# Kernel optimization log

Hardware: AMD Instinct MI355X
Metric: run time of the kernel (lower is better)

The kernel has to match this reference:

```python
import jax, jax.numpy as jnp
import numpy as np
from functools import partial

ALPHA = 0.99   # EMA smoothing factor of unbiasedExponentialSmoother
EPS = 1e-5

def setup_inputs() -> dict:
    key = jax.random.key(0)
    B, C, T = 8, 256, 16384
    x = jax.random.normal(key, (B, C, T), dtype=jnp.float32)
    return {"x": x}

def _causal_unbiased_ema_norm(x, alpha, eps):
    # x: [B, C, T]. Causal instance norm: per (b, c) lane, running unbiased
    # EMA estimates of mean and second moment over time, then normalize.
    B, C, T = x.shape
    xt = jnp.transpose(x, (2, 0, 1))  # [T, B, C] time-major for scan

    def step(carry, xi):
        s1, s2, w = carry
        s1 = alpha * s1 + (1.0 - alpha) * xi          # EMA of x
        s2 = alpha * s2 + (1.0 - alpha) * xi * xi     # EMA of x^2
        w = alpha * w + (1.0 - alpha)                 # bias correction 1-alpha^t
        mean = s1 / w
        var = s2 / w - mean * mean
        out = (xi - mean) * jax.lax.rsqrt(var + eps)
        return (s1, s2, w), out

    z = jnp.zeros((B, C), dtype=x.dtype)
    w0 = jnp.zeros((), dtype=x.dtype)
    _, yt = jax.lax.scan(step, (z, z, w0), xt)
    return jnp.transpose(yt, (1, 2, 0))  # back to [B, C, T]

def reference(x):
    # MyInstanceNorm1d(causal=True, use_unbiasEMA=True, affine=False):
    # permute/unsqueeze wrapper around the causal unbiased-EMA smoother.
    return _causal_unbiased_ema_norm(x, ALPHA, EPS)
```

## Files before the change

kernel.cpp:

```cpp
#include <hip/hip_runtime.h>

#define T_LEN  16384
#define CHUNK  16
#define NTHR   1024
#define NWAVE  (NTHR / 64)

__global__ __launch_bounds__(NTHR, 2)
void ema_norm_kernel(const float* __restrict__ x, float* __restrict__ y) {
    const float A    = 0.99f;
    const float OMA  = (float)(1.0 - 0.99);
    const float EPSF = 1e-5f;
    const float Kf = (float)((double)((float)(1.0 - 0.99)) / (1.0 - (double)0.99f));

    const int row  = blockIdx.x;
    const int tid  = threadIdx.x;
    const int lane = tid & 63;
    const int wid  = tid >> 6;

    const float4* __restrict__ xr =
        reinterpret_cast<const float4*>(x + (size_t)row * T_LEN + (size_t)tid * CHUNK);
    float4* __restrict__ yr =
        reinterpret_cast<float4*>(y + (size_t)row * T_LEN + (size_t)tid * CHUNK);

    float4 xv[4];
#pragma unroll
    for (int i = 0; i < 4; ++i) xv[i] = xr[i];

    float s1 = 0.f, s2 = 0.f;
#pragma unroll
    for (int i = 0; i < 4; ++i) {
        float t;
        t = OMA * xv[i].x; s1 = fmaf(A, s1, t); s2 = fmaf(A, s2, t * xv[i].x);
        t = OMA * xv[i].y; s1 = fmaf(A, s1, t); s2 = fmaf(A, s2, t * xv[i].y);
        t = OMA * xv[i].z; s1 = fmaf(A, s1, t); s2 = fmaf(A, s2, t * xv[i].z);
        t = OMA * xv[i].w; s1 = fmaf(A, s1, t); s2 = fmaf(A, s2, t * xv[i].w);
    }

    float a16 = A;
#pragma unroll
    for (int i = 0; i < 4; ++i) a16 *= a16;
    float d[10];
    d[0] = a16;
#pragma unroll
    for (int k = 1; k < 10; ++k) d[k] = d[k - 1] * d[k - 1];

    float v1 = s1, v2 = s2;
#pragma unroll
    for (int k = 0; k < 6; ++k) {
        const int off = 1 << k;
        float o1 = __shfl_up(v1, off, 64);
        float o2 = __shfl_up(v2, off, 64);
        if (lane >= off) { v1 = fmaf(d[k], o1, v1); v2 = fmaf(d[k], o2, v2); }
    }
    float c1 = __shfl_up(v1, 1, 64);
    float c2 = __shfl_up(v2, 1, 64);
    if (lane == 0) { c1 = 0.f; c2 = 0.f; }

    __shared__ float tot1[NWAVE], tot2[NWAVE];
    if (lane == 63) { tot1[wid] = v1; tot2[wid] = v2; }
    __syncthreads();
    float W1 = 0.f, W2 = 0.f;
    const float Dw = d[6];
    for (int v = 0; v < wid; ++v) {
        W1 = fmaf(W1, Dw, tot1[v]);
        W2 = fmaf(W2, Dw, tot2[v]);
    }
    float fdec = 1.f;
#pragma unroll
    for (int k = 0; k < 6; ++k) if (lane & (1 << k)) fdec *= d[k];
    c1 = fmaf(W1, fdec, c1);
    c2 = fmaf(W2, fdec, c2);

    float pw = 1.f;
#pragma unroll
    for (int k = 0; k < 10; ++k) if (tid & (1 << k)) pw *= d[k];
    float wrun = (tid == 0) ? 0.f : Kf * (1.f - pw);

    s1 = c1; s2 = c2;
#pragma unroll
    for (int i = 0; i < 4; ++i) {
        float4 xq = xv[i];
        float4 oq;
        {   float xi = xq.x; float t = OMA * xi;
            s1 = fmaf(A, s1, t); s2 = fmaf(A, s2, t * xi);
            wrun = fmaf(A, wrun, OMA);
            float invw = 1.0f / wrun;
            float mean = s1 * invw;
            float var  = fmaf(-mean, mean, s2 * invw);
            float rs   = __builtin_amdgcn_rsqf(var + EPSF);
            oq.x = (xi - mean) * rs; }
        {   float xi = xq.y; float t = OMA * xi;
            s1 = fmaf(A, s1, t); s2 = fmaf(A, s2, t * xi);
            wrun = fmaf(A, wrun, OMA);
            float invw = 1.0f / wrun;
            float mean = s1 * invw;
            float var  = fmaf(-mean, mean, s2 * invw);
            float rs   = __builtin_amdgcn_rsqf(var + EPSF);
            oq.y = (xi - mean) * rs; }
        {   float xi = xq.z; float t = OMA * xi;
            s1 = fmaf(A, s1, t); s2 = fmaf(A, s2, t * xi);
            wrun = fmaf(A, wrun, OMA);
            float invw = 1.0f / wrun;
            float mean = s1 * invw;
            float var  = fmaf(-mean, mean, s2 * invw);
            float rs   = __builtin_amdgcn_rsqf(var + EPSF);
            oq.z = (xi - mean) * rs; }
        {   float xi = xq.w; float t = OMA * xi;
            s1 = fmaf(A, s1, t); s2 = fmaf(A, s2, t * xi);
            wrun = fmaf(A, wrun, OMA);
            float invw = 1.0f / wrun;
            float mean = s1 * invw;
            float var  = fmaf(-mean, mean, s2 * invw);
            float rs   = __builtin_amdgcn_rsqf(var + EPSF);
            oq.w = (xi - mean) * rs; }
        yr[i] = oq;
    }
}

extern "C" void kernel_launch(void* const* d_in, const int* in_sizes, int n_in,
                              void* d_out, int out_size, void* d_ws, size_t ws_size,
                              hipStream_t stream) {
    const float* x = (const float*)d_in[0];
    float* y = (float*)d_out;
    const int rows = in_sizes[0] / T_LEN;
    ema_norm_kernel<<<rows, NTHR, 0, stream>>>(x, y);
}
```

Baseline: 239.3 us.

## Process two half-row segments per thread and drop per-step division

Each thread now handles two 16-element chunks, one in each half of the row, with 512-thread blocks instead of 1024. The wave-total carry for the second half is chained across both halves. The output formula is rewritten algebraically as (x*w - s1) * rsqrt(s2*w - s1^2 + eps*w^2), which removes the per-element reciprocal of the running weight. This cuts ALU cost and raises independent work per thread, at the cost of more registers and a longer serial cross-wave loop.

```diff
diff --git a/kernel.cpp b/kernel.cpp
--- a/kernel.cpp
+++ b/kernel.cpp
@@ -1,39 +1,77 @@
 #include <hip/hip_runtime.h>
 
 #define T_LEN  16384
-#define CHUNK  16
-#define NTHR   1024
+#define SUB    16
+#define NTHR   512
 #define NWAVE  (NTHR / 64)
+#define HALF   (T_LEN / 2)
 
-__global__ __launch_bounds__(NTHR, 2)
-void ema_norm_kernel(const float* __restrict__ x, float* __restrict__ y) {
+
+__device__ __forceinline__ void process16(const float4* __restrict__ xv,
+                                          float4* __restrict__ yv,
+                                          float s1, float s2, float w) {
     const float A    = 0.99f;
     const float OMA  = (float)(1.0 - 0.99);
     const float EPSF = 1e-5f;
-    const float Kf = (float)((double)((float)(1.0 - 0.99)) / (1.0 - (double)0.99f));
+#pragma unroll
+    for (int i = 0; i < 4; ++i) {
+        float4 xq = xv[i];
+        float4 oq;
+#pragma unroll
+        for (int e = 0; e < 4; ++e) {
+            float xi = (e == 0) ? xq.x : (e == 1) ? xq.y : (e == 2) ? xq.z : xq.w;
+            float t = OMA * xi;
+            s1 = fmaf(A, s1, t);
+            s2 = fmaf(A, s2, t * xi);
+            w  = fmaf(A, w, OMA);
+            float w2    = w * w;
+            float numer = fmaf(xi, w, -s1);
+            float arg   = fmaf(s2, w, fmaf(-s1, s1, EPSF * w2));
+            float rs    = __builtin_amdgcn_rsqf(arg);
+            float o     = numer * rs;
+            if (e == 0) oq.x = o; else if (e == 1) oq.y = o; else if (e == 2) oq.z = o; else oq.w = o;
+        }
+        yv[i] = oq;
+    }
+}
+
+__global__ __launch_bounds__(NTHR, 6)
+void ema_norm_kernel(const float* __restrict__ x, float* __restrict__ y) {
+    const float A   = 0.99f;
+    const float OMA = (float)(1.0 - 0.99);
+    const float Kf  = (float)((double)((float)(1.0 - 0.99)) / (1.0 - (double)0.99f));
 
     const int row  = blockIdx.x;
     const int tid  = threadIdx.x;
     const int lane = tid & 63;
     const int wid  = tid >> 6;
 
-    const float4* __restrict__ xr =
-        reinterpret_cast<const float4*>(x + (size_t)row * T_LEN + (size_t)tid * CHUNK);
-    float4* __restrict__ yr =
-        reinterpret_cast<float4*>(y + (size_t)row * T_LEN + (size_t)tid * CHUNK);
+    const float* __restrict__ rowx = x + (size_t)row * T_LEN;
+    float*       __restrict__ rowy = y + (size_t)row * T_LEN;
 
-    float4 xv[4];
+    const float4* __restrict__ xrA = reinterpret_cast<const float4*>(rowx + tid * SUB);
+    const float4* __restrict__ xrB = reinterpret_cast<const float4*>(rowx + HALF + tid * SUB);
+    float4* __restrict__ yrA = reinterpret_cast<float4*>(rowy + tid * SUB);
+    float4* __restrict__ yrB = reinterpret_cast<float4*>(rowy + HALF + tid * SUB);
+
+    float4 xvA[4], xvB[4];
 #pragma unroll
-    for (int i = 0; i < 4; ++i) xv[i] = xr[i];
+    for (int i = 0; i < 4; ++i) xvA[i] = xrA[i];
+#pragma unroll
+    for (int i = 0; i < 4; ++i) xvB[i] = xrB[i];
 
-    float s1 = 0.f, s2 = 0.f;
+    float sA1 = 0.f, sA2 = 0.f, sB1 = 0.f, sB2 = 0.f;
 #pragma unroll
     for (int i = 0; i < 4; ++i) {
         float t;
-        t = OMA * xv[i].x; s1 = fmaf(A, s1, t); s2 = fmaf(A, s2, t * xv[i].x);
-        t = OMA * xv[i].y; s1 = fmaf(A, s1, t); s2 = fmaf(A, s2, t * xv[i].y);
-        t = OMA * xv[i].z; s1 = fmaf(A, s1, t); s2 = fmaf(A, s2, t * xv[i].z);
-        t = OMA * xv[i].w; s1 = fmaf(A, s1, t); s2 = fmaf(A, s2, t * xv[i].w);
+        t = OMA * xvA[i].x; sA1 = fmaf(A, sA1, t); sA2 = fmaf(A, sA2, t * xvA[i].x);
+        t = OMA * xvA[i].y; sA1 = fmaf(A, sA1, t); sA2 = fmaf(A, sA2, t * xvA[i].y);
+        t = OMA * xvA[i].z; sA1 = fmaf(A, sA1, t); sA2 = fmaf(A, sA2, t * xvA[i].z);
+        t = OMA * xvA[i].w; sA1 = fmaf(A, sA1, t); sA2 = fmaf(A, sA2, t * xvA[i].w);
+        t = OMA * xvB[i].x; sB1 = fmaf(A, sB1, t); sB2 = fmaf(A, sB2, t * xvB[i].x);
+        t = OMA * xvB[i].y; sB1 = fmaf(A, sB1, t); sB2 = fmaf(A, sB2, t * xvB[i].y);
+        t = OMA * xvB[i].z; sB1 = fmaf(A, sB1, t); sB2 = fmaf(A, sB2, t * xvB[i].z);
+        t = OMA * xvB[i].w; sB1 = fmaf(A, sB1, t); sB2 = fmaf(A, sB2, t * xvB[i].w);
     }
 
     float a16 = A;
@@ -44,77 +82,66 @@
 #pragma unroll
     for (int k = 1; k < 10; ++k) d[k] = d[k - 1] * d[k - 1];
 
-    float v1 = s1, v2 = s2;
+    float vA1 = sA1, vA2 = sA2, vB1 = sB1, vB2 = sB2;
 #pragma unroll
     for (int k = 0; k < 6; ++k) {
         const int off = 1 << k;
-        float o1 = __shfl_up(v1, off, 64);
-        float o2 = __shfl_up(v2, off, 64);
-        if (lane >= off) { v1 = fmaf(d[k], o1, v1); v2 = fmaf(d[k], o2, v2); }
+        float oA1 = __shfl_up(vA1, off, 64);
+        float oA2 = __shfl_up(vA2, off, 64);
+        float oB1 = __shfl_up(vB1, off, 64);
+        float oB2 = __shfl_up(vB2, off, 64);
+        if (lane >= off) {
+            vA1 = fmaf(d[k], oA1, vA1); vA2 = fmaf(d[k], oA2, vA2);
+            vB1 = fmaf(d[k], oB1, vB1); vB2 = fmaf(d[k], oB2, vB2);
+        }
     }
-    float c1 = __shfl_up(v1, 1, 64);
-    float c2 = __shfl_up(v2, 1, 64);
-    if (lane == 0) { c1 = 0.f; c2 = 0.f; }
+    float cA1 = __shfl_up(vA1, 1, 64);
+    float cA2 = __shfl_up(vA2, 1, 64);
+    float cB1 = __shfl_up(vB1, 1, 64);
+    float cB2 = __shfl_up(vB2, 1, 64);
+    if (lane == 0) { cA1 = 0.f; cA2 = 0.f; cB1 = 0.f; cB2 = 0.f; }
 
-    __shared__ float tot1[NWAVE], tot2[NWAVE];
-    if (lane == 63) { tot1[wid] = v1; tot2[wid] = v2; }
+    __shared__ float tA1[NWAVE], tA2[NWAVE], tB1[NWAVE], tB2[NWAVE];
+    if (lane == 63) { tA1[wid] = vA1; tA2[wid] = vA2; tB1[wid] = vB1; tB2[wid] = vB2; }
     __syncthreads();
-    float W1 = 0.f, W2 = 0.f;
+
     const float Dw = d[6];
+    float WA1 = 0.f, WA2 = 0.f;
     for (int v = 0; v < wid; ++v) {
-        W1 = fmaf(W1, Dw, tot1[v]);
-        W2 = fmaf(W2, Dw, tot2[v]);
+        WA1 = fmaf(WA1, Dw, tA1[v]);
+        WA2 = fmaf(WA2, Dw, tA2[v]);
+    }
+    float WB1 = WA1, WB2 = WA2;
+    for (int v = wid; v < NWAVE; ++v) {
+        WB1 = fmaf(WB1, Dw, tA1[v]);
+        WB2 = fmaf(WB2, Dw, tA2[v]);
+    }
+    for (int v = 0; v < wid; ++v) {
+        WB1 = fmaf(WB1, Dw, tB1[v]);
+        WB2 = fmaf(WB2, Dw, tB2[v]);
     }
     float fdec = 1.f;
 #pragma unroll
     for (int k = 0; k < 6; ++k) if (lane & (1 << k)) fdec *= d[k];
-    c1 = fmaf(W1, fdec, c1);
-    c2 = fmaf(W2, fdec, c2);
+    cA1 = fmaf(WA1, fdec, cA1);
+    cA2 = fmaf(WA2, fdec, cA2);
+    cB1 = fmaf(WB1, fdec, cB1);
+    cB2 = fmaf(WB2, fdec, cB2);
 
-    float pw = 1.f;
+    float pwA = 1.f;
 #pragma unroll
-    for (int k = 0; k < 10; ++k) if (tid & (1 << k)) pw *= d[k];
-    float wrun = (tid == 0) ? 0.f : Kf * (1.f - pw);
+    for (int k = 0; k < 9; ++k) if (tid & (1 << k)) pwA *= d[k];
+    float w0A = (tid == 0) ? 0.f : Kf * (1.f - pwA);
+    float pwB = pwA * d[9];
+    float w0B = Kf * (1.f - pwB);
 
-    s1 = c1; s2 = c2;
+    float4 ovA[4], ovB[4];
+    process16(xvA, ovA, cA1, cA2, w0A);
+    process16(xvB, ovB, cB1, cB2, w0B);
 #pragma unroll
-    for (int i = 0; i < 4; ++i) {
-        float4 xq = xv[i];
-        float4 oq;
-        {   float xi = xq.x; float t = OMA * xi;
-            s1 = fmaf(A, s1, t); s2 = fmaf(A, s2, t * xi);
-            wrun = fmaf(A, wrun, OMA);
-            float invw = 1.0f / wrun;
-            float mean = s1 * invw;
-            float var  = fmaf(-mean, mean, s2 * invw);
-            float rs   = __builtin_amdgcn_rsqf(var + EPSF);
-            oq.x = (xi - mean) * rs; }
-        {   float xi = xq.y; float t = OMA * xi;
-            s1 = fmaf(A, s1, t); s2 = fmaf(A, s2, t * xi);
-            wrun = fmaf(A, wrun, OMA);
-            float invw = 1.0f / wrun;
-            float mean = s1 * invw;
-            float var  = fmaf(-mean, mean, s2 * invw);
-            float rs   = __builtin_amdgcn_rsqf(var + EPSF);
-            oq.y = (xi - mean) * rs; }
-        {   float xi = xq.z; float t = OMA * xi;
-            s1 = fmaf(A, s1, t); s2 = fmaf(A, s2, t * xi);
-            wrun = fmaf(A, wrun, OMA);
-            float invw = 1.0f / wrun;
-            float mean = s1 * invw;
-            float var  = fmaf(-mean, mean, s2 * invw);
-            float rs   = __builtin_amdgcn_rsqf(var + EPSF);
-            oq.z = (xi - mean) * rs; }
-        {   float xi = xq.w; float t = OMA * xi;
-            s1 = fmaf(A, s1, t); s2 = fmaf(A, s2, t * xi);
-            wrun = fmaf(A, wrun, OMA);
-            float invw = 1.0f / wrun;
-            float mean = s1 * invw;
-            float var  = fmaf(-mean, mean, s2 * invw);
-            float rs   = __builtin_amdgcn_rsqf(var + EPSF);
-            oq.w = (xi - mean) * rs; }
-        yr[i] = oq;
-    }
+    for (int i = 0; i < 4; ++i) yrA[i] = ovA[i];
+#pragma unroll
+    for (int i = 0; i < 4; ++i) yrB[i] = ovB[i];
 }
 
 extern "C" void kernel_launch(void* const* d_in, const int* in_sizes, int n_in,
```

Result: slower. 301.1 us (+25.8%).

## Split rows into overlapping segments with LDS-staged coalesced I/O and division-free normalize

Applied to the files above, without the earlier changes.

Each time row is split into four segments, each handled by its own 384-thread block. A block recomputes the scan over a 2048-element warm-up window taken from before its segment, so its EMA state is correct to within alpha^2048. Global loads and stores now go through padded shared memory so they are coalesced. The per-element division is folded into a single rsq by scaling the numerator and variance by w, and block IDs are swizzled. In exchange, blocks read 1.5x the input and run extra scan work, plus two more barriers.

```diff
diff --git a/kernel.cpp b/kernel.cpp
--- a/kernel.cpp
+++ b/kernel.cpp
@@ -1,30 +1,75 @@
 #include <hip/hip_runtime.h>
 
 #define T_LEN  16384
-#define CHUNK  16
-#define NTHR   1024
-#define NWAVE  (NTHR / 64)
+#define NTHR   384
+#define NWAVE  6
+#define SEGS   4
+#define TOT4   1536
+#define PAD4(i) ((i) + ((i) >> 4))
 
-__global__ __launch_bounds__(NTHR, 2)
-void ema_norm_kernel(const float* __restrict__ x, float* __restrict__ y) {
+
+__device__ __forceinline__ void process16(const float4* __restrict__ xv,
+                                          float4* __restrict__ yv,
+                                          float s1, float s2, float w) {
     const float A    = 0.99f;
     const float OMA  = (float)(1.0 - 0.99);
     const float EPSF = 1e-5f;
-    const float Kf = (float)((double)((float)(1.0 - 0.99)) / (1.0 - (double)0.99f));
+#pragma unroll
+    for (int i = 0; i < 4; ++i) {
+        float4 xq = xv[i];
+        float4 oq;
+#pragma unroll
+        for (int e = 0; e < 4; ++e) {
+            float xi = (e == 0) ? xq.x : (e == 1) ? xq.y : (e == 2) ? xq.z : xq.w;
+            float t = OMA * xi;
+            s1 = fmaf(A, s1, t);
+            s2 = fmaf(A, s2, t * xi);
+            w  = fmaf(A, w, OMA);
+            float numer = fmaf(xi, w, -s1);
+            float arg   = fmaf(s2, w, fmaf(-s1, s1, EPSF * (w * w)));
+            float rs    = __builtin_amdgcn_rsqf(arg);
+            float o     = numer * rs;
+            if (e == 0) oq.x = o; else if (e == 1) oq.y = o; else if (e == 2) oq.z = o; else oq.w = o;
+        }
+        yv[i] = oq;
+    }
+}
 
-    const int row  = blockIdx.x;
+__global__ __launch_bounds__(NTHR, 8)
+void ema_norm_kernel(const float* __restrict__ x, float* __restrict__ y) {
+    const float A   = 0.99f;
+    const float OMA = (float)(1.0 - 0.99);
+    const float Kf  = (float)((double)((float)(1.0 - 0.99)) / (1.0 - (double)0.99f));
+
+    const int o   = (blockIdx.x & 7) * 1024 + (blockIdx.x >> 3);
+    const int row = o >> 2;
+    const int seg = o & 3;
+
     const int tid  = threadIdx.x;
     const int lane = tid & 63;
     const int wid  = tid >> 6;
 
-    const float4* __restrict__ xr =
-        reinterpret_cast<const float4*>(x + (size_t)row * T_LEN + (size_t)tid * CHUNK);
-    float4* __restrict__ yr =
-        reinterpret_cast<float4*>(y + (size_t)row * T_LEN + (size_t)tid * CHUNK);
+    const float4* __restrict__ xr4 = reinterpret_cast<const float4*>(x + (size_t)row * T_LEN);
+    float4*       __restrict__ yr4 = reinterpret_cast<float4*>(y + (size_t)row * T_LEN);
+
+    __shared__ float4 buf[TOT4 + TOT4 / 16];
+    __shared__ float  tW1[NWAVE], tW2[NWAVE];
+
+    const int base4 = seg * 1024 - 512;
+
+#pragma unroll
+    for (int k = 0; k < 4; ++k) {
+        int i = tid + NTHR * k;
+        int g = base4 + i;
+        float4 v = make_float4(0.f, 0.f, 0.f, 0.f);
+        if (g >= 0) v = xr4[g];
+        buf[PAD4(i)] = v;
+    }
+    __syncthreads();
 
     float4 xv[4];
 #pragma unroll
-    for (int i = 0; i < 4; ++i) xv[i] = xr[i];
+    for (int c = 0; c < 4; ++c) { int i = 4 * tid + c; xv[c] = buf[PAD4(i)]; }
 
     float s1 = 0.f, s2 = 0.f;
 #pragma unroll
@@ -56,14 +101,13 @@
     float c2 = __shfl_up(v2, 1, 64);
     if (lane == 0) { c1 = 0.f; c2 = 0.f; }
 
-    __shared__ float tot1[NWAVE], tot2[NWAVE];
-    if (lane == 63) { tot1[wid] = v1; tot2[wid] = v2; }
+    if (lane == 63) { tW1[wid] = v1; tW2[wid] = v2; }
     __syncthreads();
     float W1 = 0.f, W2 = 0.f;
     const float Dw = d[6];
     for (int v = 0; v < wid; ++v) {
-        W1 = fmaf(W1, Dw, tot1[v]);
-        W2 = fmaf(W2, Dw, tot2[v]);
+        W1 = fmaf(W1, Dw, tW1[v]);
+        W2 = fmaf(W2, Dw, tW2[v]);
     }
     float fdec = 1.f;
 #pragma unroll
@@ -71,49 +115,28 @@
     c1 = fmaf(W1, fdec, c1);
     c2 = fmaf(W2, fdec, c2);
 
-    float pw = 1.f;
+    const int m = 256 * seg - 128 + tid;
+    float w0 = 0.f;
+    if (m > 0) {
+        float pw = 1.f;
 #pragma unroll
-    for (int k = 0; k < 10; ++k) if (tid & (1 << k)) pw *= d[k];
-    float wrun = (tid == 0) ? 0.f : Kf * (1.f - pw);
+        for (int k = 0; k < 10; ++k) if (m & (1 << k)) pw *= d[k];
+        w0 = Kf * (1.f - pw);
+    }
 
-    s1 = c1; s2 = c2;
+    float4 ov[4];
+    process16(xv, ov, c1, c2, w0);
 #pragma unroll
-    for (int i = 0; i < 4; ++i) {
-        float4 xq = xv[i];
-        float4 oq;
-        {   float xi = xq.x; float t = OMA * xi;
-            s1 = fmaf(A, s1, t); s2 = fmaf(A, s2, t * xi);
-            wrun = fmaf(A, wrun, OMA);
-            float invw = 1.0f / wrun;
-            float mean = s1 * invw;
-            float var  = fmaf(-mean, mean, s2 * invw);
-            float rs   = __builtin_amdgcn_rsqf(var + EPSF);
-            oq.x = (xi - mean) * rs; }
-        {   float xi = xq.y; float t = OMA * xi;
-            s1 = fmaf(A, s1, t); s2 = fmaf(A, s2, t * xi);
-            wrun = fmaf(A, wrun, OMA);
-            float invw = 1.0f / wrun;
-            float mean = s1 * invw;
-            float var  = fmaf(-mean, mean, s2 * invw);
-            float rs   = __builtin_amdgcn_rsqf(var + EPSF);
-            oq.y = (xi - mean) * rs; }
-        {   float xi = xq.z; float t = OMA * xi;
-            s1 = fmaf(A, s1, t); s2 = fmaf(A, s2, t * xi);
-            wrun = fmaf(A, wrun, OMA);
-            float invw = 1.0f / wrun;
-            float mean = s1 * invw;
-            float var  = fmaf(-mean, mean, s2 * invw);
-            float rs   = __builtin_amdgcn_rsqf(var + EPSF);
-            oq.z = (xi - mean) * rs; }
-        {   float xi = xq.w; float t = OMA * xi;
-            s1 = fmaf(A, s1, t); s2 = fmaf(A, s2, t * xi);
-            wrun = fmaf(A, wrun, OMA);
-            float invw = 1.0f / wrun;
-            float mean = s1 * invw;
-            float var  = fmaf(-mean, mean, s2 * invw);
-            float rs   = __builtin_amdgcn_rsqf(var + EPSF);
-            oq.w = (xi - mean) * rs; }
-        yr[i] = oq;
+    for (int c = 0; c < 4; ++c) { int i = 4 * tid + c; buf[PAD4(i)] = ov[c]; }
+    __syncthreads();
+
+#pragma unroll
+    for (int k = 0; k < 3; ++k) {
+        int i = tid + NTHR * k;
+        if (i < 1024) {
+            int s = 512 + i;
+            yr4[seg * 1024 + i] = buf[PAD4(s)];
+        }
     }
 }
 
@@ -123,5 +146,5 @@
     const float* x = (const float*)d_in[0];
     float* y = (float*)d_out;
     const int rows = in_sizes[0] / T_LEN;
-    ema_norm_kernel<<<rows, NTHR, 0, stream>>>(x, y);
+    ema_norm_kernel<<<rows * SEGS, NTHR, 0, stream>>>(x, y);
 }
```

Result: faster. 233.4 us (-2.5%).
